# Kernel tuning notes

Measured on AMD Instinct MI355X. Metric: run time of the kernel, lower is better.

Reference implementation:

```python
import jax, jax.numpy as jnp
import numpy as np

NUM_HEADS = 8

def setup_inputs() -> dict:
    key = jax.random.key(0)
    k1, k2, k3, k4 = jax.random.split(key, 4)
    B, N, C = 2, 4096, 768
    x = jax.random.normal(k1, (B, N, C), dtype=jnp.float32)
    w_qkv = jax.random.normal(k2, (C, 3 * C), dtype=jnp.float32) * (C ** -0.5)
    w_proj = jax.random.normal(k3, (C, C), dtype=jnp.float32) * (C ** -0.5)
    b_proj = jax.random.normal(k4, (C,), dtype=jnp.float32) * 0.02
    return {"x": x, "w_qkv": w_qkv, "w_proj": w_proj, "b_proj": b_proj}

def reference(x, w_qkv, w_proj, b_proj):
    B, N, C = x.shape
    H = NUM_HEADS
    Dh = C // H
    scale = Dh ** -0.5
    # qkv: [B, N, 3C] -> [B, N, 3, H, Dh] -> [3, B, H, N, Dh]
    qkv = (x @ w_qkv).reshape(B, N, 3, H, Dh).transpose(2, 0, 3, 1, 4)
    q, k, v = qkv[0], qkv[1], qkv[2]
    attn = jnp.einsum('bhqd,bhkd->bhqk', q, k) * scale  # [B,H,N,N]
    attn = jax.nn.softmax(attn, axis=-1)
    out = jnp.einsum('bhqk,bhkd->bhqd', attn, v)        # [B,H,N,Dh]
    out = out.transpose(0, 2, 1, 3).reshape(B, N, C)
    return out @ w_proj + b_proj
```

## Files before the change

kernel.cpp:

```cpp
#include <hip/hip_runtime.h>
#include <hip/hip_bf16.h>

typedef __attribute__((ext_vector_type(8))) short short8;
typedef __attribute__((ext_vector_type(4))) short short4v;
typedef __attribute__((ext_vector_type(4))) float f32x4;
typedef __attribute__((ext_vector_type(16))) float f32x16;

#define MFMA16(a,b,c) __builtin_amdgcn_mfma_f32_16x16x32_bf16(a,b,c,0,0,0)
#define MFMA32(a,b,c) __builtin_amdgcn_mfma_f32_32x32x16_bf16(a,b,c,0,0,0)

__device__ __forceinline__ unsigned short f2b_rne(float f){
  union { float f; unsigned int u; } v; v.f = f;
  unsigned int u = v.u;
  return (unsigned short)((u + 0x7FFFu + ((u >> 16) & 1u)) >> 16);
}

__device__ __forceinline__ f32x16 zero16(){
  f32x16 z;
  #pragma unroll
  for (int i = 0; i < 16; ++i) z[i] = 0.f;
  return z;
}

__global__ __launch_bounds__(256) void k_cvt(const float* __restrict__ in,
                                             unsigned short* __restrict__ out, int n8){
  int i = blockIdx.x * 256 + threadIdx.x;
  if (i >= n8) return;
  const float4* p = (const float4*)in + (size_t)i * 2;
  float4 a = p[0], b = p[1];
  short8 o;
  o[0] = (short)f2b_rne(a.x); o[1] = (short)f2b_rne(a.y);
  o[2] = (short)f2b_rne(a.z); o[3] = (short)f2b_rne(a.w);
  o[4] = (short)f2b_rne(b.x); o[5] = (short)f2b_rne(b.y);
  o[6] = (short)f2b_rne(b.z); o[7] = (short)f2b_rne(b.w);
  *((short8*)out + i) = o;
}

__global__ void k_transpose_cvt(const float* __restrict__ in, unsigned short* __restrict__ out,
                                int R, int Cc){
  __shared__ unsigned short tile[32][33];
  int c0 = blockIdx.x * 32, r0 = blockIdx.y * 32;
  int tx = threadIdx.x, ty = threadIdx.y;
  #pragma unroll
  for (int i = 0; i < 32; i += 8)
    tile[ty + i][tx] = f2b_rne(in[(size_t)(r0 + ty + i) * Cc + c0 + tx]);
  __syncthreads();
  #pragma unroll
  for (int i = 0; i < 32; i += 8)
    out[(size_t)(c0 + ty + i) * R + r0 + tx] = tile[tx][ty + i];
}

__global__ __launch_bounds__(256) void k_gemm_qkv(
    const unsigned short* __restrict__ A,
    const unsigned short* __restrict__ Bt,
    unsigned short* __restrict__ qbuf,
    unsigned short* __restrict__ kbuf,
    unsigned short* __restrict__ vtb)
{
  __shared__ short As[128 * 40];
  __shared__ short Bs[128 * 40];
  int m0 = blockIdx.x * 128, n0 = blockIdx.y * 128;
  int t = threadIdx.x, l = t & 63, w = t >> 6;
  int lr = l & 15, lh = l >> 4;
  int wr = w >> 1, wc = w & 1;

  int row0 = t >> 2, cs0 = t & 3;
  int row1 = row0 + 64;
  const unsigned short* ga0 = A  + (size_t)(m0 + row0) * 768 + cs0 * 8;
  const unsigned short* ga1 = A  + (size_t)(m0 + row1) * 768 + cs0 * 8;
  const unsigned short* gb0 = Bt + (size_t)(n0 + row0) * 768 + cs0 * 8;
  const unsigned short* gb1 = Bt + (size_t)(n0 + row1) * 768 + cs0 * 8;
  short* la0 = As + row0 * 40 + cs0 * 8;
  short* la1 = As + row1 * 40 + cs0 * 8;
  short* lb0 = Bs + row0 * 40 + cs0 * 8;
  short* lb1 = Bs + row1 * 40 + cs0 * 8;

  f32x4 acc[4][4];
  f32x4 z4 = {0.f, 0.f, 0.f, 0.f};
  #pragma unroll
  for (int mf = 0; mf < 4; ++mf)
    #pragma unroll
    for (int nf = 0; nf < 4; ++nf) acc[mf][nf] = z4;

  short8 ra0 = *(const short8*)ga0;
  short8 ra1 = *(const short8*)ga1;
  short8 rb0 = *(const short8*)gb0;
  short8 rb1 = *(const short8*)gb1;

  for (int kt = 0; kt < 24; ++kt){
    __syncthreads();
    *(short8*)la0 = ra0; *(short8*)la1 = ra1;
    *(short8*)lb0 = rb0; *(short8*)lb1 = rb1;
    __syncthreads();
    if (kt < 23){
      ra0 = *(const short8*)(ga0 + (kt + 1) * 32);
      ra1 = *(const short8*)(ga1 + (kt + 1) * 32);
      rb0 = *(const short8*)(gb0 + (kt + 1) * 32);
      rb1 = *(const short8*)(gb1 + (kt + 1) * 32);
    }
    short8 af[4], bfm[4];
    #pragma unroll
    for (int mf = 0; mf < 4; ++mf)
      af[mf] = *(const short8*)(As + (wr * 64 + mf * 16 + lr) * 40 + lh * 8);
    #pragma unroll
    for (int nf = 0; nf < 4; ++nf)
      bfm[nf] = *(const short8*)(Bs + (wc * 64 + nf * 16 + lr) * 40 + lh * 8);
    #pragma unroll
    for (int mf = 0; mf < 4; ++mf)
      #pragma unroll
      for (int nf = 0; nf < 4; ++nf)
        acc[mf][nf] = MFMA16(af[mf], bfm[nf], acc[mf][nf]);
  }

  const float qscale = 0.10206207261596577f * 1.4426950408889634f;
  int three = n0 / 768;
  int b_ = m0 >> 12;
  int ntok0 = m0 & 4095;
  #pragma unroll
  for (int nf = 0; nf < 4; ++nf){
    int gcol = n0 + wc * 64 + nf * 16 + lr;
    int jj = gcol - three * 768;
    int h = jj / 96;
    int dh = jj - h * 96;
    #pragma unroll
    for (int mf = 0; mf < 4; ++mf){
      int ntok = ntok0 + wr * 64 + mf * 16 + lh * 4;
      if (three == 0){
        unsigned short* dst = qbuf + (size_t)(b_ * 8 + h) * 4096 * 96;
        #pragma unroll
        for (int r = 0; r < 4; ++r)
          dst[(size_t)(ntok + r) * 96 + dh] = f2b_rne(acc[mf][nf][r] * qscale);
      } else if (three == 1){
        unsigned short* dst = kbuf + (size_t)(b_ * 8 + h) * 4096 * 96;
        #pragma unroll
        for (int r = 0; r < 4; ++r)
          dst[(size_t)(ntok + r) * 96 + dh] = f2b_rne(acc[mf][nf][r]);
      } else {
        short4v sv;
        #pragma unroll
        for (int r = 0; r < 4; ++r) sv[r] = (short)f2b_rne(acc[mf][nf][r]);
        *(short4v*)(vtb + ((size_t)(b_ * 8 + h) * 96 + dh) * 4096 + ntok) = sv;
      }
    }
  }
}

__global__ __launch_bounds__(512) void k_attn12(
    const unsigned short* __restrict__ qb,
    const unsigned short* __restrict__ kb,
    const unsigned short* __restrict__ vtb,
    unsigned short* __restrict__ ao)
{
  __shared__ short lds[27136];
  const int bh = blockIdx.x;
  const int qt = blockIdx.y;
  const int tid = threadIdx.x;
  const int ln = tid & 63, wid = tid >> 6;
  const int qc = ln & 31, hi = ln >> 5;
  const int q0 = qt * 256 + wid * 32;

  const unsigned short* qbase = qb  + (size_t)bh * 4096 * 96;
  const unsigned short* kbase = kb  + (size_t)bh * 4096 * 96;
  const unsigned short* vbase = vtb + (size_t)bh * 96 * 4096;

  short8 qf[6];
  #pragma unroll
  for (int kw = 0; kw < 6; ++kw)
    qf[kw] = *(const short8*)(qbase + (size_t)(q0 + qc) * 96 + kw * 16 + hi * 8);

  const unsigned short* gp[3]; int gstep[3], loff[3], lstep[3];
  #pragma unroll
  for (int j = 0; j < 3; ++j){
    int c = tid + j * 512;
    if (c < 768){
      int r = c / 12, cl = c - r * 12;
      gp[j] = kbase + r * 96 + cl * 8; gstep[j] = 64 * 96;
      loff[j] = r * 104 + cl * 8;      lstep[j] = 6656;
    } else {
      int cv = c - 768; int r = cv >> 3, cl = cv & 7;
      gp[j] = vbase + (size_t)r * 4096 + cl * 8; gstep[j] = 64;
      loff[j] = 13312 + r * 72 + cl * 8;         lstep[j] = 6912;
    }
  }

  short8 rs[3];
  #pragma unroll
  for (int j = 0; j < 3; ++j){ rs[j] = *(const short8*)gp[j]; gp[j] += gstep[j]; }
  #pragma unroll
  for (int j = 0; j < 3; ++j) *(short8*)(lds + loff[j]) = rs[j];

  f32x16 oacc[3];
  #pragma unroll
  for (int dt = 0; dt < 3; ++dt) oacc[dt] = zero16();
  float lsum = 0.f;

  const int krd = qc * 104 + hi * 8;
  const int vrd = 13312 + qc * 72 + hi * 8;

#define CVTPK(d, lo_, hi_) asm("v_cvt_pk_bf16_f32 %0, %1, %2" : "=v"(d) : "v"(lo_), "v"(hi_))
#define PLSWAP(x_, y_)     asm("v_permlane32_swap_b32 %0, %1" : "+v"(x_), "+v"(y_))

  for (int kt = 0; kt < 64; ++kt){
    const int cur = kt & 1;
    __syncthreads();
    if (kt < 63){
      #pragma unroll
      for (int j = 0; j < 3; ++j){ rs[j] = *(const short8*)gp[j]; gp[j] += gstep[j]; }
    }
    const short* Kb = lds + cur * 6656 + krd;
    const short* Vb = lds + cur * 6912 + vrd;

    f32x16 s0 = zero16(), s1 = zero16();
    __builtin_amdgcn_s_setprio(1);
    #pragma unroll
    for (int kw = 0; kw < 6; ++kw){
      short8 kf = *(const short8*)(Kb + kw * 16);
      s0 = MFMA32(kf, qf[kw], s0);
    }
    #pragma unroll
    for (int kw = 0; kw < 6; ++kw){
      short8 kf = *(const short8*)(Kb + 3328 + kw * 16);
      s1 = MFMA32(kf, qf[kw], s1);
    }
    __builtin_amdgcn_s_setprio(0);

    {
      float p0 = 0.f, p1 = 0.f, p2 = 0.f, p3 = 0.f;
      #pragma unroll
      for (int r = 0; r < 16; r += 4){
        s0[r]   = exp2f(s0[r]   - 12.0f); p0 += s0[r];
        s0[r+1] = exp2f(s0[r+1] - 12.0f); p1 += s0[r+1];
        s0[r+2] = exp2f(s0[r+2] - 12.0f); p2 += s0[r+2];
        s0[r+3] = exp2f(s0[r+3] - 12.0f); p3 += s0[r+3];
      }
      #pragma unroll
      for (int r = 0; r < 16; r += 4){
        s1[r]   = exp2f(s1[r]   - 12.0f); p0 += s1[r];
        s1[r+1] = exp2f(s1[r+1] - 12.0f); p1 += s1[r+1];
        s1[r+2] = exp2f(s1[r+2] - 12.0f); p2 += s1[r+2];
        s1[r+3] = exp2f(s1[r+3] - 12.0f); p3 += s1[r+3];
      }
      lsum += (p0 + p1) + (p2 + p3);
    }

    short8 pa[4];
    {
      unsigned int a, b;
      union { unsigned int u[4]; short8 s; } pk;
      CVTPK(a, s0[0], s0[1]);  CVTPK(b, s0[4],  s0[5]);  PLSWAP(a, b); pk.u[0] = a; pk.u[2] = b;
      CVTPK(a, s0[2], s0[3]);  CVTPK(b, s0[6],  s0[7]);  PLSWAP(a, b); pk.u[1] = a; pk.u[3] = b;
      pa[0] = pk.s;
      CVTPK(a, s0[8], s0[9]);  CVTPK(b, s0[12], s0[13]); PLSWAP(a, b); pk.u[0] = a; pk.u[2] = b;
      CVTPK(a, s0[10], s0[11]); CVTPK(b, s0[14], s0[15]); PLSWAP(a, b); pk.u[1] = a; pk.u[3] = b;
      pa[1] = pk.s;
      CVTPK(a, s1[0], s1[1]);  CVTPK(b, s1[4],  s1[5]);  PLSWAP(a, b); pk.u[0] = a; pk.u[2] = b;
      CVTPK(a, s1[2], s1[3]);  CVTPK(b, s1[6],  s1[7]);  PLSWAP(a, b); pk.u[1] = a; pk.u[3] = b;
      pa[2] = pk.s;
      CVTPK(a, s1[8], s1[9]);  CVTPK(b, s1[12], s1[13]); PLSWAP(a, b); pk.u[0] = a; pk.u[2] = b;
      CVTPK(a, s1[10], s1[11]); CVTPK(b, s1[14], s1[15]); PLSWAP(a, b); pk.u[1] = a; pk.u[3] = b;
      pa[3] = pk.s;
    }

    __builtin_amdgcn_s_setprio(1);
    #pragma unroll
    for (int dt = 0; dt < 3; ++dt){
      #pragma unroll
      for (int w = 0; w < 4; ++w){
        short8 vf = *(const short8*)(Vb + dt * 2304 + w * 16);
        oacc[dt] = MFMA32(vf, pa[w], oacc[dt]);
      }
    }
    __builtin_amdgcn_s_setprio(0);

    if (kt < 63){
      const int nb = cur ^ 1;
      #pragma unroll
      for (int j = 0; j < 3; ++j) *(short8*)(lds + loff[j] + nb * lstep[j]) = rs[j];
    }
  }

  float lt = lsum + __shfl_xor(lsum, 32, 64);
  float inv = 1.0f / lt;
  int b_ = bh >> 3, h = bh & 7;
  unsigned short* orow = ao + (size_t)(b_ * 4096 + q0 + qc) * 768 + h * 96;
  #pragma unroll
  for (int dt = 0; dt < 3; ++dt)
    #pragma unroll
    for (int g = 0; g < 4; ++g){
      short4v sv;
      #pragma unroll
      for (int r = 0; r < 4; ++r) sv[r] = (short)f2b_rne(oacc[dt][g * 4 + r] * inv);
      *(short4v*)(orow + dt * 32 + g * 8 + hi * 4) = sv;
    }
#undef CVTPK
#undef PLSWAP
}

__global__ __launch_bounds__(256) void k_gemm_proj(
    const unsigned short* __restrict__ A,
    const unsigned short* __restrict__ Bt,
    const float* __restrict__ bias,
    float* __restrict__ out)
{
  __shared__ short As[128 * 40];
  __shared__ short Bs[128 * 40];
  int m0 = blockIdx.x * 128, n0 = blockIdx.y * 128;
  int t = threadIdx.x, l = t & 63, w = t >> 6;
  int lr = l & 15, lh = l >> 4;
  int wr = w >> 1, wc = w & 1;

  int row0 = t >> 2, cs0 = t & 3;
  int row1 = row0 + 64;
  const unsigned short* ga0 = A  + (size_t)(m0 + row0) * 768 + cs0 * 8;
  const unsigned short* ga1 = A  + (size_t)(m0 + row1) * 768 + cs0 * 8;
  const unsigned short* gb0 = Bt + (size_t)(n0 + row0) * 768 + cs0 * 8;
  const unsigned short* gb1 = Bt + (size_t)(n0 + row1) * 768 + cs0 * 8;
  short* la0 = As + row0 * 40 + cs0 * 8;
  short* la1 = As + row1 * 40 + cs0 * 8;
  short* lb0 = Bs + row0 * 40 + cs0 * 8;
  short* lb1 = Bs + row1 * 40 + cs0 * 8;

  f32x4 acc[4][4];
  f32x4 z4 = {0.f, 0.f, 0.f, 0.f};
  #pragma unroll
  for (int mf = 0; mf < 4; ++mf)
    #pragma unroll
    for (int nf = 0; nf < 4; ++nf) acc[mf][nf] = z4;

  short8 ra0 = *(const short8*)ga0;
  short8 ra1 = *(const short8*)ga1;
  short8 rb0 = *(const short8*)gb0;
  short8 rb1 = *(const short8*)gb1;

  for (int kt = 0; kt < 24; ++kt){
    __syncthreads();
    *(short8*)la0 = ra0; *(short8*)la1 = ra1;
    *(short8*)lb0 = rb0; *(short8*)lb1 = rb1;
    __syncthreads();
    if (kt < 23){
      ra0 = *(const short8*)(ga0 + (kt + 1) * 32);
      ra1 = *(const short8*)(ga1 + (kt + 1) * 32);
      rb0 = *(const short8*)(gb0 + (kt + 1) * 32);
      rb1 = *(const short8*)(gb1 + (kt + 1) * 32);
    }
    short8 af[4], bfm[4];
    #pragma unroll
    for (int mf = 0; mf < 4; ++mf)
      af[mf] = *(const short8*)(As + (wr * 64 + mf * 16 + lr) * 40 + lh * 8);
    #pragma unroll
    for (int nf = 0; nf < 4; ++nf)
      bfm[nf] = *(const short8*)(Bs + (wc * 64 + nf * 16 + lr) * 40 + lh * 8);
    #pragma unroll
    for (int mf = 0; mf < 4; ++mf)
      #pragma unroll
      for (int nf = 0; nf < 4; ++nf)
        acc[mf][nf] = MFMA16(af[mf], bfm[nf], acc[mf][nf]);
  }

  #pragma unroll
  for (int nf = 0; nf < 4; ++nf){
    int gcol = n0 + wc * 64 + nf * 16 + lr;
    float bb = bias[gcol];
    #pragma unroll
    for (int mf = 0; mf < 4; ++mf){
      int grow = m0 + wr * 64 + mf * 16 + lh * 4;
      #pragma unroll
      for (int r = 0; r < 4; ++r)
        out[(size_t)(grow + r) * 768 + gcol] = acc[mf][nf][r] + bb;
    }
  }
}

extern "C" void kernel_launch(void* const* d_in, const int* in_sizes, int n_in,
                              void* d_out, int out_size, void* d_ws, size_t ws_size,
                              hipStream_t stream) {
  const float* x      = (const float*)d_in[0];
  const float* w_qkv  = (const float*)d_in[1];
  const float* w_proj = (const float*)d_in[2];
  const float* b_proj = (const float*)d_in[3];
  float* out = (float*)d_out;
  char* ws = (char*)d_ws;

  unsigned short* xb     = (unsigned short*)(ws);
  unsigned short* wqkvt  = (unsigned short*)(ws + 12582912);
  unsigned short* wprojt = (unsigned short*)(ws + 16121856);
  unsigned short* qbuf   = (unsigned short*)(ws + 17301504);
  unsigned short* kbuf   = (unsigned short*)(ws + 29884416);
  unsigned short* vtb    = (unsigned short*)(ws + 42467328);
  unsigned short* aob    = xb;

  k_cvt<<<3072, 256, 0, stream>>>(x, xb, 786432);
  k_transpose_cvt<<<dim3(72, 24), dim3(32, 8), 0, stream>>>(w_qkv, wqkvt, 768, 2304);
  k_transpose_cvt<<<dim3(24, 24), dim3(32, 8), 0, stream>>>(w_proj, wprojt, 768, 768);
  k_gemm_qkv<<<dim3(64, 18), 256, 0, stream>>>(xb, wqkvt, qbuf, kbuf, vtb);
  k_attn12<<<dim3(16, 16), 512, 0, stream>>>(qbuf, kbuf, vtb, aob);
  k_gemm_proj<<<dim3(64, 6), 256, 0, stream>>>(aob, wprojt, b_proj, out);
}
```

Measured before the change: 216.4 us.

## Split attention KV range across two wave sets and reduce partial outputs in LDS

The attention kernel now handles 128 queries per block instead of 256, and the waves form two sets. Each set processes alternating halves of every 128-key chunk, so the grid doubles to 512 blocks. The point is better occupancy and CU fill across the 256 CUs. The double-buffered LDS is replaced by one stage with two barriers per iteration, so load/compute overlap is reduced. Partial accumulators and row sums from the second set are merged through LDS at the end. This appears valid only because softmax uses a fixed max (no running max), which makes the partial sums additive.

```diff
diff --git a/kernel.cpp b/kernel.cpp
--- a/kernel.cpp
+++ b/kernel.cpp
@@ -145,7 +145,7 @@
   }
 }
 
-__global__ __launch_bounds__(512) void k_attn12(
+__global__ __launch_bounds__(512) void k_attn13(
     const unsigned short* __restrict__ qb,
     const unsigned short* __restrict__ kb,
     const unsigned short* __restrict__ vtb,
@@ -157,7 +157,8 @@
   const int tid = threadIdx.x;
   const int ln = tid & 63, wid = tid >> 6;
   const int qc = ln & 31, hi = ln >> 5;
-  const int q0 = qt * 256 + wid * 32;
+  const int set = wid >> 2, qquad = wid & 3;
+  const int q0 = qt * 128 + qquad * 32;
 
   const unsigned short* qbase = qb  + (size_t)bh * 4096 * 96;
   const unsigned short* kbase = kb  + (size_t)bh * 4096 * 96;
@@ -168,47 +169,56 @@
   for (int kw = 0; kw < 6; ++kw)
     qf[kw] = *(const short8*)(qbase + (size_t)(q0 + qc) * 96 + kw * 16 + hi * 8);
 
-  const unsigned short* gp[3]; int gstep[3], loff[3], lstep[3];
+  const unsigned short* gp[6]; int loff[6];
   #pragma unroll
   for (int j = 0; j < 3; ++j){
-    int c = tid + j * 512;
-    if (c < 768){
-      int r = c / 12, cl = c - r * 12;
-      gp[j] = kbase + r * 96 + cl * 8; gstep[j] = 64 * 96;
-      loff[j] = r * 104 + cl * 8;      lstep[j] = 6656;
-    } else {
-      int cv = c - 768; int r = cv >> 3, cl = cv & 7;
-      gp[j] = vbase + (size_t)r * 4096 + cl * 8; gstep[j] = 64;
-      loff[j] = 13312 + r * 72 + cl * 8;         lstep[j] = 6912;
-    }
-  }
-
-  short8 rs[3];
-  #pragma unroll
-  for (int j = 0; j < 3; ++j){ rs[j] = *(const short8*)gp[j]; gp[j] += gstep[j]; }
-  #pragma unroll
-  for (int j = 0; j < 3; ++j) *(short8*)(lds + loff[j]) = rs[j];
+    int ck = tid + j * 512;
+    int s = (ck >= 768) ? 1 : 0;
+    int cc = ck - s * 768;
+    int r = cc / 12, cl = cc - r * 12;
+    gp[j] = kbase + (size_t)(s * 64 + r) * 96 + cl * 8;
+    loff[j] = s * 6656 + r * 104 + cl * 8;
+  }
+  #pragma unroll
+  for (int j = 3; j < 6; ++j){
+    int cv = tid + (j - 3) * 512;
+    int s = (cv >= 768) ? 1 : 0;
+    int cc = cv - s * 768;
+    int r = cc >> 3, cl = cc & 7;
+    gp[j] = vbase + (size_t)r * 4096 + s * 64 + cl * 8;
+    loff[j] = 13312 + s * 6912 + r * 72 + cl * 8;
+  }
+
+  short8 rs[6];
+  #pragma unroll
+  for (int j = 0; j < 6; ++j) rs[j] = *(const short8*)gp[j];
+  #pragma unroll
+  for (int j = 0; j < 3; ++j) gp[j] += 12288;
+  #pragma unroll
+  for (int j = 3; j < 6; ++j) gp[j] += 128;
+  #pragma unroll
+  for (int j = 0; j < 6; ++j) *(short8*)(lds + loff[j]) = rs[j];
 
   f32x16 oacc[3];
   #pragma unroll
   for (int dt = 0; dt < 3; ++dt) oacc[dt] = zero16();
   float lsum = 0.f;
 
-  const int krd = qc * 104 + hi * 8;
-  const int vrd = 13312 + qc * 72 + hi * 8;
+  const short* Kb = lds + set * 6656 + qc * 104 + hi * 8;
+  const short* Vb = lds + 13312 + set * 6912 + qc * 72 + hi * 8;
 
 #define CVTPK(d, lo_, hi_) asm("v_cvt_pk_bf16_f32 %0, %1, %2" : "=v"(d) : "v"(lo_), "v"(hi_))
 #define PLSWAP(x_, y_)     asm("v_permlane32_swap_b32 %0, %1" : "+v"(x_), "+v"(y_))
 
-  for (int kt = 0; kt < 64; ++kt){
-    const int cur = kt & 1;
-    __syncthreads();
-    if (kt < 63){
-      #pragma unroll
-      for (int j = 0; j < 3; ++j){ rs[j] = *(const short8*)gp[j]; gp[j] += gstep[j]; }
-    }
-    const short* Kb = lds + cur * 6656 + krd;
-    const short* Vb = lds + cur * 6912 + vrd;
+  for (int ss = 0; ss < 32; ++ss){
+    __syncthreads();
+
+    if (ss < 31){
+      #pragma unroll
+      for (int j = 0; j < 3; ++j){ rs[j] = *(const short8*)gp[j]; gp[j] += 12288; }
+      #pragma unroll
+      for (int j = 3; j < 6; ++j){ rs[j] = *(const short8*)gp[j]; gp[j] += 128; }
+    }
 
     f32x16 s0 = zero16(), s1 = zero16();
     __builtin_amdgcn_s_setprio(1);
@@ -272,26 +282,50 @@
     }
     __builtin_amdgcn_s_setprio(0);
 
-    if (kt < 63){
-      const int nb = cur ^ 1;
-      #pragma unroll
-      for (int j = 0; j < 3; ++j) *(short8*)(lds + loff[j] + nb * lstep[j]) = rs[j];
-    }
-  }
-
-  float lt = lsum + __shfl_xor(lsum, 32, 64);
-  float inv = 1.0f / lt;
-  int b_ = bh >> 3, h = bh & 7;
-  unsigned short* orow = ao + (size_t)(b_ * 4096 + q0 + qc) * 768 + h * 96;
-  #pragma unroll
-  for (int dt = 0; dt < 3; ++dt)
-    #pragma unroll
-    for (int g = 0; g < 4; ++g){
-      short4v sv;
-      #pragma unroll
-      for (int r = 0; r < 4; ++r) sv[r] = (short)f2b_rne(oacc[dt][g * 4 + r] * inv);
-      *(short4v*)(orow + dt * 32 + g * 8 + hi * 4) = sv;
-    }
+    __syncthreads();
+    if (ss < 31){
+      #pragma unroll
+      for (int j = 0; j < 6; ++j) *(short8*)(lds + loff[j]) = rs[j];
+    }
+  }
+
+  float* fl = (float*)lds;
+  {
+    __syncthreads();
+    if (set == 1){
+      #pragma unroll
+      for (int dt = 0; dt < 3; ++dt)
+        #pragma unroll
+        for (int r = 0; r < 16; ++r)
+          fl[qquad * 3072 + dt * 1024 + r * 64 + ln] = oacc[dt][r];
+      fl[12288 + qquad * 64 + ln] = lsum;
+    }
+    __syncthreads();
+    if (set == 0){
+      lsum += fl[12288 + qquad * 64 + ln];
+      #pragma unroll
+      for (int dt = 0; dt < 3; ++dt)
+        #pragma unroll
+        for (int r = 0; r < 16; ++r)
+          oacc[dt][r] += fl[qquad * 3072 + dt * 1024 + r * 64 + ln];
+    }
+  }
+
+  if (set == 0){
+    float lt = lsum + __shfl_xor(lsum, 32, 64);
+    float inv = 1.0f / lt;
+    int b_ = bh >> 3, h = bh & 7;
+    unsigned short* orow = ao + (size_t)(b_ * 4096 + q0 + qc) * 768 + h * 96;
+    #pragma unroll
+    for (int dt = 0; dt < 3; ++dt)
+      #pragma unroll
+      for (int g4 = 0; g4 < 4; ++g4){
+        short4v sv;
+        #pragma unroll
+        for (int r = 0; r < 4; ++r) sv[r] = (short)f2b_rne(oacc[dt][g4 * 4 + r] * inv);
+        *(short4v*)(orow + dt * 32 + g4 * 8 + hi * 4) = sv;
+      }
+  }
 #undef CVTPK
 #undef PLSWAP
 }
@@ -393,6 +427,6 @@
   k_transpose_cvt<<<dim3(72, 24), dim3(32, 8), 0, stream>>>(w_qkv, wqkvt, 768, 2304);
   k_transpose_cvt<<<dim3(24, 24), dim3(32, 8), 0, stream>>>(w_proj, wprojt, 768, 768);
   k_gemm_qkv<<<dim3(64, 18), 256, 0, stream>>>(xb, wqkvt, qbuf, kbuf, vtb);
-  k_attn12<<<dim3(16, 16), 512, 0, stream>>>(qbuf, kbuf, vtb, aob);
+  k_attn13<<<dim3(16, 32), 512, 0, stream>>>(qbuf, kbuf, vtb, aob);
   k_gemm_proj<<<dim3(64, 6), 256, 0, stream>>>(aob, wprojt, b_proj, out);
 }
```

New measurement: 246.4 us. 13.9% more time.
